# Kernel tuning notes

Hardware: AMD Instinct MI355X
Metric: run time of the kernel (lower is better)

Reference implementation:

```python
import jax, jax.numpy as jnp
import numpy as np

N_NODES = 100000


def setup_inputs() -> dict:
    key = jax.random.key(0)
    k1, k2, k3, k4, k5, k6 = jax.random.split(key, 6)
    x = jax.random.normal(k1, (N_NODES, 256), dtype=jnp.float32)
    edge_index = jax.random.randint(k2, (2, 3200000), 0, N_NODES, dtype=jnp.int64)
    # GCNConv(256, 3): glorot weight + zero bias (PyG default)
    lim1 = float(np.sqrt(6.0 / (256 + 3)))
    W1 = jax.random.uniform(k3, (256, 3), minval=-lim1, maxval=lim1, dtype=jnp.float32)
    b1 = jnp.zeros((3,), dtype=jnp.float32)
    # Linear(3, 7): torch default kaiming-uniform-ish bounds
    lim2 = float(1.0 / np.sqrt(3))
    W2 = jax.random.uniform(k4, (3, 7), minval=-lim2, maxval=lim2, dtype=jnp.float32)
    b2 = jax.random.uniform(k5, (7,), minval=-lim2, maxval=lim2, dtype=jnp.float32)
    return {"x": x, "edge_index": edge_index, "W1": W1, "b1": b1, "W2": W2, "b2": b2}


def gcn_conv(x, edge_index, W, b, num_nodes):
    # PyG GCNConv: add self-loops, symmetric deg^-1/2 (A+I) deg^-1/2 normalization,
    # aggregate transformed features, then add bias.
    loop = jnp.arange(num_nodes, dtype=edge_index.dtype)
    src = jnp.concatenate([edge_index[0], loop])
    dst = jnp.concatenate([edge_index[1], loop])
    ones = jnp.ones_like(dst, dtype=x.dtype)
    deg = jax.ops.segment_sum(ones, dst, num_segments=num_nodes)  # [N]
    dinv = jnp.where(deg > 0, jax.lax.rsqrt(deg), 0.0)
    norm = dinv[src] * dinv[dst]  # [E+N]
    h = x @ W  # [N, 3] — transform BEFORE gather (small width)
    msg = h[src] * norm[:, None]  # [E+N, 3]
    agg = jax.ops.segment_sum(msg, dst, num_segments=num_nodes)  # [N, 3]
    return agg + b


def reference(x, edge_index, W1, b1, W2, b2):
    h = jax.nn.relu(gcn_conv(x, edge_index, W1, b1, x.shape[0]))  # [N, 3]
    z = h @ W2 + b2  # [N, 7]
    return (h, z)
```

## Files before the change

### kernel.cpp

```cpp
#include <hip/hip_runtime.h>
#include <stdint.h>


#define BSHIFT 8
#define BNODES 256
#define BPAD 392
#define CAPM 16384
#define SPLITC 8
#define NBX 1024

__device__ __forceinline__ bool ei_is64(const unsigned* __restrict__ ei) {
    const int t = threadIdx.x;
    const int nz = (t < 256) && (ei[2 * t + 1] != 0u);
    return __syncthreads_or(nz) == 0;
}

__global__ __launch_bounds__(512) void k_pre(const float* __restrict__ x,
                                             const float* __restrict__ W1,
                                             float4* __restrict__ part4,
                                             const unsigned* __restrict__ ei,
                                             unsigned* __restrict__ cnt_tbl,
                                             int E, int B, int CH, int nbin, int N) {
    const bool is64 = ei_is64(ei);
    if ((int)blockIdx.x < nbin) {
        __shared__ unsigned cnt[BPAD];
        for (int i = threadIdx.x; i < BPAD; i += 512) cnt[i] = 0u;
        __syncthreads();
        const int e0 = blockIdx.x * CH;
        const int e1 = min(E, e0 + CH);
        if (is64) {
            const uint4* dp = (const uint4*)(ei + 2 * (size_t)E + 2 * e0);
            const int n2 = (e1 - e0) >> 1;
            for (int q = threadIdx.x; q < n2; q += 512) {
                const uint4 v = dp[q];
                atomicAdd(&cnt[v.x >> BSHIFT], 1u);
                atomicAdd(&cnt[v.z >> BSHIFT], 1u);
            }
            for (int e = e0 + 2 * n2 + threadIdx.x; e < e1; e += 512)
                atomicAdd(&cnt[ei[2 * (size_t)E + 2 * e] >> BSHIFT], 1u);
        } else {
            const uint4* dp = (const uint4*)(ei + (size_t)E + e0);
            const int n4 = (e1 - e0) >> 2;
            for (int q = threadIdx.x; q < n4; q += 512) {
                const uint4 v = dp[q];
                atomicAdd(&cnt[v.x >> BSHIFT], 1u);
                atomicAdd(&cnt[v.y >> BSHIFT], 1u);
                atomicAdd(&cnt[v.z >> BSHIFT], 1u);
                atomicAdd(&cnt[v.w >> BSHIFT], 1u);
            }
            for (int e = e0 + 4 * n4 + threadIdx.x; e < e1; e += 512)
                atomicAdd(&cnt[ei[(size_t)E + e] >> BSHIFT], 1u);
        }
        __syncthreads();
        for (int i = threadIdx.x; i < B; i += 512)
            cnt_tbl[(size_t)blockIdx.x * BPAD + i] = cnt[i];
    } else {
        const int bx     = blockIdx.x - nbin;
        const int gtid   = bx * 512 + threadIdx.x;
        const int nwaves = (((int)gridDim.x - nbin) * 512) >> 6;
        const int wave   = gtid >> 6;
        const int lane   = threadIdx.x & 63;
        const int fg     = lane & 15;
        const int m      = lane >> 4;
        const int f      = wave & 3;
        const int wq     = wave >> 2;
        const int wstep  = nwaves >> 2;
        float w[4][3];
#pragma unroll
        for (int j = 0; j < 4; ++j)
#pragma unroll
            for (int c = 0; c < 3; ++c)
                w[j][c] = W1[(f * 64 + fg * 4 + j) * 3 + c];
        const int nq = (N + 3) >> 2;
        for (int q = wq; q < nq; q += 4 * wstep) {
            int nd[4]; bool ok[4]; float4 v[4];
#pragma unroll
            for (int u = 0; u < 4; ++u) {
                const int qu = q + u * wstep;
                nd[u] = qu * 4 + m;
                ok[u] = (qu < nq) && (nd[u] < N);
                v[u]  = ok[u] ? *reinterpret_cast<const float4*>(
                                    x + (size_t)nd[u] * 256 + f * 64 + fg * 4)
                              : make_float4(0.f, 0.f, 0.f, 0.f);
            }
#pragma unroll
            for (int u = 0; u < 4; ++u) {
                float s0 = v[u].x * w[0][0] + v[u].y * w[1][0] + v[u].z * w[2][0] + v[u].w * w[3][0];
                float s1 = v[u].x * w[0][1] + v[u].y * w[1][1] + v[u].z * w[2][1] + v[u].w * w[3][1];
                float s2 = v[u].x * w[0][2] + v[u].y * w[1][2] + v[u].z * w[2][2] + v[u].w * w[3][2];
#pragma unroll
                for (int off = 8; off >= 1; off >>= 1) {
                    s0 += __shfl_xor(s0, off, 64);
                    s1 += __shfl_xor(s1, off, 64);
                    s2 += __shfl_xor(s2, off, 64);
                }
                if (ok[u] && fg == 0)
                    part4[(size_t)f * N + nd[u]] = make_float4(s0, s1, s2, 0.f);
            }
        }
    }
}

__global__ __launch_bounds__(512) void k_prefix(const unsigned* __restrict__ cnt_tbl,
                                                unsigned* __restrict__ base_tbl,
                                                unsigned* __restrict__ total,
                                                int nbin) {
    __shared__ unsigned arr[512];
    const int bb = blockIdx.x;
    const int t  = threadIdx.x;
    const unsigned c = (t < nbin) ? cnt_tbl[(size_t)t * BPAD + bb] : 0u;
    arr[t] = c;
    __syncthreads();
#pragma unroll
    for (int off = 1; off < 512; off <<= 1) {
        const unsigned v = (t >= off) ? arr[t - off] : 0u;
        __syncthreads();
        arr[t] += v;
        __syncthreads();
    }
    if (t < nbin) base_tbl[(size_t)t * BPAD + bb] = arr[t] - c;
    if (t == 511) total[bb] = arr[511];
}

__global__ __launch_bounds__(512) void k_scatter(const unsigned* __restrict__ ei,
                                                 const unsigned* __restrict__ base_tbl,
                                                 unsigned* __restrict__ records,
                                                 int E, int B, int CH) {
    const bool is64 = ei_is64(ei);
    __shared__ unsigned gbase[BPAD], cur[BPAD];
    const int j = blockIdx.x;
    for (int i = threadIdx.x; i < B; i += 512) {
        gbase[i] = (unsigned)i * CAPM + base_tbl[(size_t)j * BPAD + i];
        cur[i]   = 0u;
    }
    __syncthreads();
    const int e0 = j * CH;
    const int e1 = min(E, e0 + CH);

    auto emit = [&](unsigned s, unsigned d) {
        const unsigned bb  = d >> BSHIFT;
        const unsigned idx = atomicAdd(&cur[bb], 1u);
        const unsigned pos = gbase[bb] + idx;
        if (pos < (bb + 1u) * CAPM)
            records[pos] = (s << BSHIFT) | (d & (BNODES - 1));
    };

    const int nq = (e1 - e0) >> 2;
    if (is64) {
        const unsigned long long* e64 = (const unsigned long long*)ei;
        const ulonglong2* sp = (const ulonglong2*)(e64 + e0);
        const ulonglong2* dp = (const ulonglong2*)(e64 + (size_t)E + e0);
        for (int q = threadIdx.x; q < nq; q += 512) {
            const ulonglong2 sa = sp[2 * q], sb = sp[2 * q + 1];
            const ulonglong2 da = dp[2 * q], db = dp[2 * q + 1];
            emit((unsigned)sa.x, (unsigned)da.x);
            emit((unsigned)sa.y, (unsigned)da.y);
            emit((unsigned)sb.x, (unsigned)db.x);
            emit((unsigned)sb.y, (unsigned)db.y);
        }
        for (int e = e0 + 4 * nq + threadIdx.x; e < e1; e += 512)
            emit((unsigned)e64[e], (unsigned)e64[(size_t)E + e]);
    } else {
        const uint4* sp = (const uint4*)(ei + e0);
        const uint4* dp = (const uint4*)(ei + (size_t)E + e0);
        for (int q = threadIdx.x; q < nq; q += 512) {
            const uint4 s4 = sp[q], d4 = dp[q];
            emit(s4.x, d4.x);
            emit(s4.y, d4.y);
            emit(s4.z, d4.z);
            emit(s4.w, d4.w);
        }
        for (int e = e0 + 4 * nq + threadIdx.x; e < e1; e += 512)
            emit(ei[e], ei[(size_t)E + e]);
    }
}

__global__ __launch_bounds__(256) void k_cnt2(const unsigned* __restrict__ records,
                                              const unsigned* __restrict__ total,
                                              unsigned* __restrict__ pcount) {
    __shared__ unsigned cnt[BNODES];
    const int b  = blockIdx.x >> 3;
    const int sl = blockIdx.x & 7;
    cnt[threadIdx.x] = 0u;
    __syncthreads();
    int n = (int)total[b]; if (n > CAPM) n = CAPM;
    const int chunk = (n + SPLITC - 1) / SPLITC;
    const int lo = sl * chunk;
    const int hi = min(n, lo + chunk);
    const unsigned* rec = records + (size_t)b * CAPM;
    int i = lo + threadIdx.x;
    for (; i + 256 < hi; i += 512) {
        const unsigned r0 = rec[i], r1 = rec[i + 256];
        atomicAdd(&cnt[r0 & (BNODES - 1)], 1u);
        atomicAdd(&cnt[r1 & (BNODES - 1)], 1u);
    }
    if (i < hi) atomicAdd(&cnt[rec[i] & (BNODES - 1)], 1u);
    __syncthreads();
    pcount[((size_t)blockIdx.x << BSHIFT) + threadIdx.x] = cnt[threadIdx.x];
}

__global__ __launch_bounds__(256) void k_dinv2(const float4* __restrict__ part4,
                                               const unsigned* __restrict__ pcount,
                                               float* __restrict__ g4, int N) {
    const int i = blockIdx.x * 256 + threadIdx.x;
    if (i >= N) return;
    const int b = i >> BSHIFT, t = i & (BNODES - 1);
    const float4 p0 = part4[i];
    const float4 p1 = part4[(size_t)N + i];
    const float4 p2 = part4[(size_t)2 * N + i];
    const float4 p3 = part4[(size_t)3 * N + i];
    const float hx = p0.x + p1.x + p2.x + p3.x;
    const float hy = p0.y + p1.y + p2.y + p3.y;
    const float hz = p0.z + p1.z + p2.z + p3.z;
    unsigned deg = 1u;
#pragma unroll
    for (int s = 0; s < SPLITC; ++s)
        deg += pcount[(((size_t)b * SPLITC + s) << BSHIFT) + t];
    const float r = rsqrtf((float)deg);
    reinterpret_cast<float4*>(g4)[i] = make_float4(hx * r, hy * r, hz * r, r);
}

__global__ __launch_bounds__(256) void k_msg2(const unsigned* __restrict__ records,
                                              const unsigned* __restrict__ total,
                                              const float* __restrict__ g4,
                                              float* __restrict__ psum) {
    __shared__ float acc[BNODES * 3];
    const int b  = blockIdx.x >> 3;
    const int sl = blockIdx.x & 7;
    for (int i = threadIdx.x; i < BNODES * 3; i += 256) acc[i] = 0.f;
    __syncthreads();
    int n = (int)total[b]; if (n > CAPM) n = CAPM;
    const int chunk = (n + SPLITC - 1) / SPLITC;
    const int lo = sl * chunk;
    const int hi = min(n, lo + chunk);
    const unsigned* rec = records + (size_t)b * CAPM;
    const float4* g4v = reinterpret_cast<const float4*>(g4);
    int i = lo + threadIdx.x;
    for (; i + 256 < hi; i += 512) {
        const unsigned r0 = rec[i], r1 = rec[i + 256];
        const float4 ga = g4v[r0 >> BSHIFT];
        const float4 gb = g4v[r1 >> BSHIFT];
        const unsigned l0 = (r0 & (BNODES - 1)) * 3, l1 = (r1 & (BNODES - 1)) * 3;
        atomicAdd(&acc[l0 + 0], ga.x); atomicAdd(&acc[l0 + 1], ga.y); atomicAdd(&acc[l0 + 2], ga.z);
        atomicAdd(&acc[l1 + 0], gb.x); atomicAdd(&acc[l1 + 1], gb.y); atomicAdd(&acc[l1 + 2], gb.z);
    }
    if (i < hi) {
        const unsigned r0 = rec[i];
        const float4 ga = g4v[r0 >> BSHIFT];
        const unsigned l0 = (r0 & (BNODES - 1)) * 3;
        atomicAdd(&acc[l0 + 0], ga.x); atomicAdd(&acc[l0 + 1], ga.y); atomicAdd(&acc[l0 + 2], ga.z);
    }
    __syncthreads();
    const size_t base = ((size_t)blockIdx.x * 3) << BSHIFT;
    psum[base +   0 + threadIdx.x] = acc[threadIdx.x * 3 + 0];
    psum[base + 256 + threadIdx.x] = acc[threadIdx.x * 3 + 1];
    psum[base + 512 + threadIdx.x] = acc[threadIdx.x * 3 + 2];
}

__global__ __launch_bounds__(256) void k_fin(const float* __restrict__ psum,
                                             const float* __restrict__ g4,
                                             const float* __restrict__ b1,
                                             const float* __restrict__ W2,
                                             const float* __restrict__ b2,
                                             float* __restrict__ out, int N) {
    const int i = blockIdx.x * 256 + threadIdx.x;
    if (i >= N) return;
    const int b = i >> BSHIFT, t = i & (BNODES - 1);
    float a0 = 0.f, a1 = 0.f, a2 = 0.f;
#pragma unroll
    for (int s = 0; s < SPLITC; ++s) {
        const size_t base = (((size_t)b * SPLITC + s) * 3) << BSHIFT;
        a0 += psum[base + t];
        a1 += psum[base + 256 + t];
        a2 += psum[base + 512 + t];
    }
    const float4 g = reinterpret_cast<const float4*>(g4)[i];
    const float  r = g.w;
    const float h0 = fmaxf(r * (a0 + g.x) + b1[0], 0.f);
    const float h1 = fmaxf(r * (a1 + g.y) + b1[1], 0.f);
    const float h2 = fmaxf(r * (a2 + g.z) + b1[2], 0.f);
    out[3 * (size_t)i + 0] = h0;
    out[3 * (size_t)i + 1] = h1;
    out[3 * (size_t)i + 2] = h2;
    float* z = out + (size_t)3 * N;
#pragma unroll
    for (int c = 0; c < 7; ++c)
        z[7 * (size_t)i + c] = h0 * W2[c] + h1 * W2[7 + c] + h2 * W2[14 + c] + b2[c];
}

__global__ __launch_bounds__(256) void k_xw1_fb(const float* __restrict__ x,
                                                const float* __restrict__ W1,
                                                float* __restrict__ g4,
                                                unsigned* __restrict__ zptr,
                                                int nzero, int N) {
    const int gtid = blockIdx.x * 256 + threadIdx.x;
    const int nthread = gridDim.x * 256;
    for (int i = gtid; i < nzero; i += nthread) zptr[i] = 0u;
    const int lane = threadIdx.x & 63;
    float w[4][3];
#pragma unroll
    for (int k = 0; k < 4; ++k)
#pragma unroll
        for (int c = 0; c < 3; ++c) w[k][c] = W1[(lane * 4 + k) * 3 + c];
    const int wave = gtid >> 6, nwaves = nthread >> 6;
    for (int node = wave; node < N; node += nwaves) {
        const float4 v = *reinterpret_cast<const float4*>(x + (size_t)node * 256 + lane * 4);
        float s0 = v.x * w[0][0] + v.y * w[1][0] + v.z * w[2][0] + v.w * w[3][0];
        float s1 = v.x * w[0][1] + v.y * w[1][1] + v.z * w[2][1] + v.w * w[3][1];
        float s2 = v.x * w[0][2] + v.y * w[1][2] + v.z * w[2][2] + v.w * w[3][2];
#pragma unroll
        for (int off = 32; off > 0; off >>= 1) {
            s0 += __shfl_xor(s0, off, 64);
            s1 += __shfl_xor(s1, off, 64);
            s2 += __shfl_xor(s2, off, 64);
        }
        if (lane == 0)
            reinterpret_cast<float4*>(g4)[node] = make_float4(s0, s1, s2, 0.f);
    }
}
__global__ __launch_bounds__(256) void k_deg_fb(const unsigned* __restrict__ ei,
                                                float* __restrict__ deg, int E) {
    const bool is64 = ei_is64(ei);
    const int e = blockIdx.x * 256 + threadIdx.x;
    if (e >= E) return;
    const unsigned d = is64 ? (unsigned)((const unsigned long long*)ei)[(size_t)E + e]
                            : ei[(size_t)E + e];
    atomicAdd(&deg[d], 1.0f);
}
__global__ __launch_bounds__(256) void k_dinv_fb(const float* __restrict__ deg,
                                                 float* __restrict__ g4, int N) {
    const int i = blockIdx.x * 256 + threadIdx.x;
    if (i >= N) return;
    const float r = rsqrtf(1.0f + deg[i]);
    const float4 h = reinterpret_cast<const float4*>(g4)[i];
    reinterpret_cast<float4*>(g4)[i] = make_float4(h.x * r, h.y * r, h.z * r, r);
}
__global__ __launch_bounds__(256) void k_edge_fb(const unsigned* __restrict__ ei,
                                                 const float* __restrict__ g4,
                                                 float* __restrict__ u4, int E) {
    const bool is64 = ei_is64(ei);
    const int e = blockIdx.x * 256 + threadIdx.x;
    if (e >= E) return;
    unsigned s, d;
    if (is64) {
        const unsigned long long* q = (const unsigned long long*)ei;
        s = (unsigned)q[e]; d = (unsigned)q[(size_t)E + e];
    } else {
        s = ei[e]; d = ei[(size_t)E + e];
    }
    const float4 g = reinterpret_cast<const float4*>(g4)[s];
    atomicAdd(&u4[4 * (size_t)d + 0], g.x);
    atomicAdd(&u4[4 * (size_t)d + 1], g.y);
    atomicAdd(&u4[4 * (size_t)d + 2], g.z);
}
__global__ __launch_bounds__(256) void k_final_fb(const float* __restrict__ u4,
                                                  const float* __restrict__ g4,
                                                  const float* __restrict__ b1,
                                                  const float* __restrict__ W2,
                                                  const float* __restrict__ b2,
                                                  float* __restrict__ out, int N) {
    const int i = blockIdx.x * 256 + threadIdx.x;
    if (i >= N) return;
    const float4 g = reinterpret_cast<const float4*>(g4)[i];
    const float4 u = reinterpret_cast<const float4*>(u4)[i];
    const float  r = g.w;
    const float h0 = fmaxf(r * (u.x + g.x) + b1[0], 0.f);
    const float h1 = fmaxf(r * (u.y + g.y) + b1[1], 0.f);
    const float h2 = fmaxf(r * (u.z + g.z) + b1[2], 0.f);
    out[3 * (size_t)i + 0] = h0;
    out[3 * (size_t)i + 1] = h1;
    out[3 * (size_t)i + 2] = h2;
    float* z = out + (size_t)3 * N;
#pragma unroll
    for (int c = 0; c < 7; ++c)
        z[7 * (size_t)i + c] = h0 * W2[c] + h1 * W2[7 + c] + h2 * W2[14 + c] + b2[c];
}

extern "C" void kernel_launch(void* const* d_in, const int* in_sizes, int n_in,
                              void* d_out, int out_size, void* d_ws, size_t ws_size,
                              hipStream_t stream) {
    const float*    x   = (const float*)d_in[0];
    const unsigned* ei  = (const unsigned*)d_in[1];
    const float*    W1  = (const float*)d_in[2];
    const float*    b1  = (const float*)d_in[3];
    const float*    W2  = (const float*)d_in[4];
    const float*    b2  = (const float*)d_in[5];
    float*          out = (float*)d_out;

    const int N = in_sizes[0] / 256;
    const int E = in_sizes[1] / 2;
    const int B = (N + BNODES - 1) >> BSHIFT;

    const int CH   = ((E + 381) / 382 + 3) & ~3;
    const int nbin = (E + CH - 1) / CH;

    char* ws = (char*)d_ws;
    size_t off = 256;
    float*    g4       = (float*)(ws + off);
    off = (off + 16ull * N + 255) & ~(size_t)255;
    float4*   part4    = (float4*)(ws + off);
    off = (off + 64ull * N + 255) & ~(size_t)255;
    unsigned* cnt_tbl  = (unsigned*)(ws + off);
    off = (off + 4ull * nbin * BPAD + 255) & ~(size_t)255;
    unsigned* base_tbl = (unsigned*)(ws + off);
    off = (off + 4ull * nbin * BPAD + 255) & ~(size_t)255;
    unsigned* total    = (unsigned*)(ws + off);
    off = (off + 4ull * B + 255) & ~(size_t)255;
    unsigned* pcount   = (unsigned*)(ws + off);
    float*    psum     = (float*)(ws + off);
    off = (off + 4ull * B * SPLITC * 768 + 255) & ~(size_t)255;
    unsigned* records  = (unsigned*)(ws + off);
    const size_t need  = off + 4ull * B * CAPM + 4096;

    if (ws_size >= need) {
        k_pre<<<nbin + NBX, 512, 0, stream>>>(x, W1, part4, ei, cnt_tbl, E, B, CH, nbin, N);
        k_prefix<<<B, 512, 0, stream>>>(cnt_tbl, base_tbl, total, nbin);
        k_scatter<<<nbin, 512, 0, stream>>>(ei, base_tbl, records, E, B, CH);
        k_cnt2<<<B * SPLITC, 256, 0, stream>>>(records, total, pcount);
        k_dinv2<<<(N + 255) / 256, 256, 0, stream>>>(part4, pcount, g4, N);
        k_msg2<<<B * SPLITC, 256, 0, stream>>>(records, total, g4, psum);
        k_fin<<<(N + 255) / 256, 256, 0, stream>>>(psum, g4, b1, W2, b2, out, N);
    } else {
        float* deg = (float*)part4;
        float* u4  = deg + N;
        k_xw1_fb<<<4096, 256, 0, stream>>>(x, W1, g4, (unsigned*)deg, 5 * N, N);
        k_deg_fb<<<(E + 255) / 256, 256, 0, stream>>>(ei, deg, E);
        k_dinv_fb<<<(N + 255) / 256, 256, 0, stream>>>(deg, g4, N);
        k_edge_fb<<<(E + 255) / 256, 256, 0, stream>>>(ei, g4, u4, E);
        k_final_fb<<<(N + 255) / 256, 256, 0, stream>>>(u4, g4, b1, W2, b2, out, N);
    }
}
```

Measured before the change: 123.1 us.

## Fuse bin count, prefix and scatter into one pass using global atomic bases

```diff
diff --git a/kernel.cpp b/kernel.cpp
--- a/kernel.cpp
+++ b/kernel.cpp
@@ -19,12 +19,13 @@
                                              const float* __restrict__ W1,
                                              float4* __restrict__ part4,
                                              const unsigned* __restrict__ ei,
-                                             unsigned* __restrict__ cnt_tbl,
+                                             unsigned* __restrict__ gtotal,
+                                             unsigned* __restrict__ records,
                                              int E, int B, int CH, int nbin, int N) {
     const bool is64 = ei_is64(ei);
     if ((int)blockIdx.x < nbin) {
-        __shared__ unsigned cnt[BPAD];
-        for (int i = threadIdx.x; i < BPAD; i += 512) cnt[i] = 0u;
+        __shared__ unsigned cnt[BPAD], base[BPAD], cur[BPAD];
+        for (int i = threadIdx.x; i < BPAD; i += 512) { cnt[i] = 0u; cur[i] = 0u; }
         __syncthreads();
         const int e0 = blockIdx.x * CH;
         const int e1 = min(E, e0 + CH);
@@ -53,7 +54,43 @@
         }
         __syncthreads();
         for (int i = threadIdx.x; i < B; i += 512)
-            cnt_tbl[(size_t)blockIdx.x * BPAD + i] = cnt[i];
+            base[i] = cnt[i] ? atomicAdd(&gtotal[i], cnt[i]) : 0u;
+        __syncthreads();
+        auto emit = [&](unsigned s, unsigned d) {
+            const unsigned bb  = d >> BSHIFT;
+            const unsigned idx = atomicAdd(&cur[bb], 1u);
+            const unsigned pos = base[bb] + idx;
+            if (pos < (unsigned)CAPM)
+                records[(size_t)bb * CAPM + pos] = (s << BSHIFT) | (d & (BNODES - 1));
+        };
+        const int nq = (e1 - e0) >> 2;
+        if (is64) {
+            const unsigned long long* e64 = (const unsigned long long*)ei;
+            const ulonglong2* sp = (const ulonglong2*)(e64 + e0);
+            const ulonglong2* dp = (const ulonglong2*)(e64 + (size_t)E + e0);
+            for (int q = threadIdx.x; q < nq; q += 512) {
+                const ulonglong2 sa = sp[2 * q], sb = sp[2 * q + 1];
+                const ulonglong2 da = dp[2 * q], db = dp[2 * q + 1];
+                emit((unsigned)sa.x, (unsigned)da.x);
+                emit((unsigned)sa.y, (unsigned)da.y);
+                emit((unsigned)sb.x, (unsigned)db.x);
+                emit((unsigned)sb.y, (unsigned)db.y);
+            }
+            for (int e = e0 + 4 * nq + threadIdx.x; e < e1; e += 512)
+                emit((unsigned)e64[e], (unsigned)e64[(size_t)E + e]);
+        } else {
+            const uint4* sp = (const uint4*)(ei + e0);
+            const uint4* dp = (const uint4*)(ei + (size_t)E + e0);
+            for (int q = threadIdx.x; q < nq; q += 512) {
+                const uint4 s4 = sp[q], d4 = dp[q];
+                emit(s4.x, d4.x);
+                emit(s4.y, d4.y);
+                emit(s4.z, d4.z);
+                emit(s4.w, d4.w);
+            }
+            for (int e = e0 + 4 * nq + threadIdx.x; e < e1; e += 512)
+                emit(ei[e], ei[(size_t)E + e]);
+        }
     } else {
         const int bx     = blockIdx.x - nbin;
         const int gtid   = bx * 512 + threadIdx.x;
@@ -98,80 +135,6 @@
                     part4[(size_t)f * N + nd[u]] = make_float4(s0, s1, s2, 0.f);
             }
         }
-    }
-}
-
-__global__ __launch_bounds__(512) void k_prefix(const unsigned* __restrict__ cnt_tbl,
-                                                unsigned* __restrict__ base_tbl,
-                                                unsigned* __restrict__ total,
-                                                int nbin) {
-    __shared__ unsigned arr[512];
-    const int bb = blockIdx.x;
-    const int t  = threadIdx.x;
-    const unsigned c = (t < nbin) ? cnt_tbl[(size_t)t * BPAD + bb] : 0u;
-    arr[t] = c;
-    __syncthreads();
-#pragma unroll
-    for (int off = 1; off < 512; off <<= 1) {
-        const unsigned v = (t >= off) ? arr[t - off] : 0u;
-        __syncthreads();
-        arr[t] += v;
-        __syncthreads();
-    }
-    if (t < nbin) base_tbl[(size_t)t * BPAD + bb] = arr[t] - c;
-    if (t == 511) total[bb] = arr[511];
-}
-
-__global__ __launch_bounds__(512) void k_scatter(const unsigned* __restrict__ ei,
-                                                 const unsigned* __restrict__ base_tbl,
-                                                 unsigned* __restrict__ records,
-                                                 int E, int B, int CH) {
-    const bool is64 = ei_is64(ei);
-    __shared__ unsigned gbase[BPAD], cur[BPAD];
-    const int j = blockIdx.x;
-    for (int i = threadIdx.x; i < B; i += 512) {
-        gbase[i] = (unsigned)i * CAPM + base_tbl[(size_t)j * BPAD + i];
-        cur[i]   = 0u;
-    }
-    __syncthreads();
-    const int e0 = j * CH;
-    const int e1 = min(E, e0 + CH);
-
-    auto emit = [&](unsigned s, unsigned d) {
-        const unsigned bb  = d >> BSHIFT;
-        const unsigned idx = atomicAdd(&cur[bb], 1u);
-        const unsigned pos = gbase[bb] + idx;
-        if (pos < (bb + 1u) * CAPM)
-            records[pos] = (s << BSHIFT) | (d & (BNODES - 1));
-    };
-
-    const int nq = (e1 - e0) >> 2;
-    if (is64) {
-        const unsigned long long* e64 = (const unsigned long long*)ei;
-        const ulonglong2* sp = (const ulonglong2*)(e64 + e0);
-        const ulonglong2* dp = (const ulonglong2*)(e64 + (size_t)E + e0);
-        for (int q = threadIdx.x; q < nq; q += 512) {
-            const ulonglong2 sa = sp[2 * q], sb = sp[2 * q + 1];
-            const ulonglong2 da = dp[2 * q], db = dp[2 * q + 1];
-            emit((unsigned)sa.x, (unsigned)da.x);
-            emit((unsigned)sa.y, (unsigned)da.y);
-            emit((unsigned)sb.x, (unsigned)db.x);
-            emit((unsigned)sb.y, (unsigned)db.y);
-        }
-        for (int e = e0 + 4 * nq + threadIdx.x; e < e1; e += 512)
-            emit((unsigned)e64[e], (unsigned)e64[(size_t)E + e]);
-    } else {
-        const uint4* sp = (const uint4*)(ei + e0);
-        const uint4* dp = (const uint4*)(ei + (size_t)E + e0);
-        for (int q = threadIdx.x; q < nq; q += 512) {
-            const uint4 s4 = sp[q], d4 = dp[q];
-            emit(s4.x, d4.x);
-            emit(s4.y, d4.y);
-            emit(s4.z, d4.z);
-            emit(s4.w, d4.w);
-        }
-        for (int e = e0 + 4 * nq + threadIdx.x; e < e1; e += 512)
-            emit(ei[e], ei[(size_t)E + e]);
     }
 }
 
@@ -391,34 +354,30 @@
     const int E = in_sizes[1] / 2;
     const int B = (N + BNODES - 1) >> BSHIFT;
 
-    const int CH   = ((E + 381) / 382 + 3) & ~3;
+    const int CH   = ((E + 255) / 256 + 3) & ~3;
     const int nbin = (E + CH - 1) / CH;
 
     char* ws = (char*)d_ws;
     size_t off = 256;
-    float*    g4       = (float*)(ws + off);
+    float*    g4      = (float*)(ws + off);
     off = (off + 16ull * N + 255) & ~(size_t)255;
-    float4*   part4    = (float4*)(ws + off);
+    float4*   part4   = (float4*)(ws + off);
     off = (off + 64ull * N + 255) & ~(size_t)255;
-    unsigned* cnt_tbl  = (unsigned*)(ws + off);
-    off = (off + 4ull * nbin * BPAD + 255) & ~(size_t)255;
-    unsigned* base_tbl = (unsigned*)(ws + off);
-    off = (off + 4ull * nbin * BPAD + 255) & ~(size_t)255;
-    unsigned* total    = (unsigned*)(ws + off);
+    unsigned* gtotal  = (unsigned*)(ws + off);
     off = (off + 4ull * B + 255) & ~(size_t)255;
-    unsigned* pcount   = (unsigned*)(ws + off);
-    float*    psum     = (float*)(ws + off);
+    unsigned* pcount  = (unsigned*)(ws + off);
+    float*    psum    = (float*)(ws + off);
     off = (off + 4ull * B * SPLITC * 768 + 255) & ~(size_t)255;
-    unsigned* records  = (unsigned*)(ws + off);
-    const size_t need  = off + 4ull * B * CAPM + 4096;
+    unsigned* records = (unsigned*)(ws + off);
+    const size_t need = off + 4ull * B * CAPM + 4096;
 
     if (ws_size >= need) {
-        k_pre<<<nbin + NBX, 512, 0, stream>>>(x, W1, part4, ei, cnt_tbl, E, B, CH, nbin, N);
-        k_prefix<<<B, 512, 0, stream>>>(cnt_tbl, base_tbl, total, nbin);
-        k_scatter<<<nbin, 512, 0, stream>>>(ei, base_tbl, records, E, B, CH);
-        k_cnt2<<<B * SPLITC, 256, 0, stream>>>(records, total, pcount);
+        hipMemsetAsync(gtotal, 0, 4ull * B, stream);
+        k_pre<<<nbin + NBX, 512, 0, stream>>>(x, W1, part4, ei, gtotal, records,
+                                              E, B, CH, nbin, N);
+        k_cnt2<<<B * SPLITC, 256, 0, stream>>>(records, gtotal, pcount);
         k_dinv2<<<(N + 255) / 256, 256, 0, stream>>>(part4, pcount, g4, N);
-        k_msg2<<<B * SPLITC, 256, 0, stream>>>(records, total, g4, psum);
+        k_msg2<<<B * SPLITC, 256, 0, stream>>>(records, gtotal, g4, psum);
         k_fin<<<(N + 255) / 256, 256, 0, stream>>>(psum, g4, b1, W2, b2, out, N);
     } else {
         float* deg = (float*)part4;
```

Measured after the change: 118.8 us. 1.04x faster.
